# Optimization experiments

Measured on AMD Instinct MI355X. Metric: run time of the kernel, lower is better.

The kernel has to match this reference:

```python
import jax, jax.numpy as jnp
import numpy as np

N_NODES = 100000
N_EDGES = 1600000
F_IN = 128
HIDDEN = 128
N_CLASSES = 32
N_GRAPHS = 64


def setup_inputs() -> dict:
    key = jax.random.key(0)
    ks = jax.random.split(key, 10)
    x = jax.random.normal(ks[0], (N_NODES, F_IN), dtype=jnp.float32)
    edge_index = jax.random.randint(ks[1], (2, N_EDGES), 0, N_NODES, dtype=jnp.int64)
    batch = jnp.sort(jax.random.randint(ks[2], (N_NODES,), 0, N_GRAPHS, dtype=jnp.int64))
    s1 = 1.0 / np.sqrt(F_IN)
    s2 = 1.0 / np.sqrt(HIDDEN)
    W1 = jax.random.normal(ks[3], (F_IN, HIDDEN), dtype=jnp.float32) * s1
    b1 = jnp.zeros((HIDDEN,), dtype=jnp.float32)
    W2 = jax.random.normal(ks[4], (HIDDEN, HIDDEN), dtype=jnp.float32) * s2
    b2 = jnp.zeros((HIDDEN,), dtype=jnp.float32)
    fcW = jax.random.normal(ks[5], (HIDDEN, N_CLASSES), dtype=jnp.float32) * s2
    fcb = jnp.zeros((N_CLASSES,), dtype=jnp.float32)
    return {"x": x, "edge_index": edge_index, "batch": batch,
            "W1": W1, "b1": b1, "W2": W2, "b2": b2, "fcW": fcW, "fcb": fcb}


def _gcn_layer(x, src, dst, W, b, num_nodes):
    # PyG GCNConv: h = X W; out = D^-1/2 (A + I) D^-1/2 h + b,
    # degrees computed over incoming edges at dst, including self-loops.
    h = x @ W  # [N, H]
    ones = jnp.ones(src.shape[0], dtype=x.dtype)
    deg = jax.ops.segment_sum(ones, dst, num_segments=num_nodes) + 1.0  # +1 self-loop
    dinv = jax.lax.rsqrt(deg)  # [N]
    enorm = dinv[src] * dinv[dst]  # [E] per-edge symmetric normalization
    agg = jax.ops.segment_sum(h[src] * enorm[:, None], dst, num_segments=num_nodes)
    agg = agg + h * (dinv * dinv)[:, None]  # self-loop message
    return agg + b


def reference(x, edge_index, batch, W1, b1, W2, b2, fcW, fcb):
    num_nodes = x.shape[0]
    src, dst = edge_index[0], edge_index[1]
    h = jax.nn.relu(_gcn_layer(x, src, dst, W1, b1, num_nodes))
    h = jax.nn.relu(_gcn_layer(h, src, dst, W2, b2, num_nodes))
    # global mean pool per graph
    sums = jax.ops.segment_sum(h, batch, num_segments=N_GRAPHS)  # [G, H]
    cnt = jax.ops.segment_sum(jnp.ones((num_nodes, 1), h.dtype), batch, num_segments=N_GRAPHS)
    pooled = sums / jnp.maximum(cnt, 1.0)
    return pooled @ fcW + fcb  # [G, C]
```

## Files before the change

### kernel.cpp

```cpp
#include <hip/hip_runtime.h>
#include <hip/hip_bf16.h>

#define N_NODES   100000
#define FDIM      128
#define N_GRAPHS  64
#define N_CLASSES 32

#define NB        ((N_NODES + 255) / 256)
#define EPB       8192
#define SCAN_CHUNK 2048

typedef __attribute__((ext_vector_type(8))) short short8;
typedef __attribute__((ext_vector_type(4))) float f32x4;

__device__ __forceinline__ float bf2f(unsigned int u16) {
    unsigned int x = u16 << 16;
    return __builtin_bit_cast(float, x);
}
__device__ __forceinline__ unsigned short f2bf(float f) {
    unsigned int u = __builtin_bit_cast(unsigned int, f);
    unsigned int r = (u + 0x7fffu + ((u >> 16) & 1u)) >> 16;
    return (unsigned short)r;
}

__global__ __launch_bounds__(256) void hist_kernel(const int* __restrict__ dst, int* __restrict__ hist,
                                                   int nE, int nblk) {
    __shared__ int h[NB];
    int t = threadIdx.x, blk = blockIdx.x;
    for (int i = t; i < NB; i += 256) h[i] = 0;
    __syncthreads();
    int base = blk * EPB;
    #pragma unroll
    for (int j = 0; j < EPB / 256; ++j) {
        int e = base + j * 256 + t;
        if (e < nE) atomicAdd(&h[dst[e] >> 8], 1);
    }
    __syncthreads();
    for (int i = t; i < NB; i += 256) hist[i * nblk + blk] = h[i];
}

__global__ __launch_bounds__(256) void scan_p1(const int* __restrict__ a, int* __restrict__ bsums, int n) {
    __shared__ int wsum[4];
    int b = blockIdx.x, t = threadIdx.x;
    int base = b * SCAN_CHUNK;
    int sum = 0;
    #pragma unroll
    for (int j = 0; j < SCAN_CHUNK / 256; ++j) {
        int idx = base + j * 256 + t;
        sum += (idx < n) ? a[idx] : 0;
    }
    #pragma unroll
    for (int off = 32; off; off >>= 1) sum += __shfl_down(sum, off, 64);
    int lane = t & 63, w = t >> 6;
    if (lane == 0) wsum[w] = sum;
    __syncthreads();
    if (t == 0) bsums[b] = wsum[0] + wsum[1] + wsum[2] + wsum[3];
}

__global__ __launch_bounds__(64) void scan_p2(int* __restrict__ bsums, int nb) {
    int t = threadIdx.x;
    int carry = 0;
    for (int base = 0; base < nb; base += 64) {
        int i = base + t;
        int v = (i < nb) ? bsums[i] : 0;
        int inc = v;
        #pragma unroll
        for (int off = 1; off < 64; off <<= 1) {
            int y = __shfl_up(inc, off, 64);
            if (t >= off) inc += y;
        }
        if (i < nb) bsums[i] = carry + inc - v;
        carry += __shfl(inc, 63, 64);
    }
}

__global__ __launch_bounds__(256) void scan_p3(const int* __restrict__ a, const int* __restrict__ bsums,
                                               int* __restrict__ out, int n) {
    __shared__ int wsum[4];
    int b = blockIdx.x, t = threadIdx.x;
    int lane = t & 63, w = t >> 6;
    int i0 = b * SCAN_CHUNK + t * 8;
    int v[8];
    int s = 0;
    #pragma unroll
    for (int j = 0; j < 8; ++j) {
        int idx = i0 + j;
        v[j] = (idx < n) ? a[idx] : 0;
        s += v[j];
    }
    int ps = s;
    #pragma unroll
    for (int off = 1; off < 64; off <<= 1) {
        int y = __shfl_up(ps, off, 64);
        if (lane >= off) ps += y;
    }
    if (lane == 63) wsum[w] = ps;
    __syncthreads();
    if (t == 0) {
        int acc = 0;
        #pragma unroll
        for (int i = 0; i < 4; ++i) { int tmp = wsum[i]; wsum[i] = acc; acc += tmp; }
    }
    __syncthreads();
    int run = (ps - s) + wsum[w] + bsums[b];
    #pragma unroll
    for (int j = 0; j < 8; ++j) {
        int idx = i0 + j;
        if (idx < n) out[idx] = run;
        run += v[j];
    }
}

__global__ __launch_bounds__(256) void part_kernel(const int* __restrict__ src, const int* __restrict__ dst,
                                                   const int* __restrict__ offs,
                                                   unsigned long long* __restrict__ recs,
                                                   int nE, int nblk) {
    __shared__ int cur[NB];
    int t = threadIdx.x, blk = blockIdx.x;
    for (int i = t; i < NB; i += 256) cur[i] = offs[i * nblk + blk];
    __syncthreads();
    int base = blk * EPB;
    #pragma unroll
    for (int j = 0; j < EPB / 256; ++j) {
        int e = base + j * 256 + t;
        if (e < nE) {
            int s = src[e], d = dst[e];
            int pos = atomicAdd(&cur[d >> 8], 1);
            recs[pos] = (unsigned long long)(unsigned)s | ((unsigned long long)(unsigned)d << 32);
        }
    }
}

__global__ __launch_bounds__(256) void csr_kernel(const unsigned long long* __restrict__ recs,
                                                  const int* __restrict__ offs,
                                                  int* __restrict__ row_ptr, int* __restrict__ esrc,
                                                  float* __restrict__ dinv, int nE, int nblk) {
    __shared__ int cnt[256];
    __shared__ int cur[256];
    __shared__ int wsum[4];
    int b = blockIdx.x, t = threadIdx.x;
    int node0 = b << 8;
    int segBeg = offs[b * nblk];
    int segEnd = (b + 1 < NB) ? offs[(b + 1) * nblk] : nE;
    cnt[t] = 0;
    __syncthreads();
    for (int e = segBeg + t; e < segEnd; e += 256) {
        int d = (int)(recs[e] >> 32);
        atomicAdd(&cnt[d - node0], 1);
    }
    __syncthreads();
    int c = cnt[t];
    int lane = t & 63, w = t >> 6;
    int ps = c;
    #pragma unroll
    for (int off = 1; off < 64; off <<= 1) {
        int y = __shfl_up(ps, off, 64);
        if (lane >= off) ps += y;
    }
    if (lane == 63) wsum[w] = ps;
    __syncthreads();
    if (t == 0) {
        int a = 0;
        #pragma unroll
        for (int i = 0; i < 4; ++i) { int tmp = wsum[i]; wsum[i] = a; a += tmp; }
    }
    __syncthreads();
    int gbase = segBeg + (ps - c) + wsum[w];
    cur[t] = gbase;
    int node = node0 + t;
    if (node < N_NODES) {
        row_ptr[node] = gbase;
        dinv[node] = rsqrtf((float)c + 1.0f);
    }
    if (b == NB - 1 && t == 0) row_ptr[N_NODES] = nE;
    __syncthreads();
    for (int e = segBeg + t; e < segEnd; e += 256) {
        unsigned long long r = recs[e];
        int d = (int)(r >> 32);
        int pos = atomicAdd(&cur[d - node0], 1);
        esrc[pos] = (int)(r & 0xffffffffu);
    }
}

__global__ __launch_bounds__(256) void wtrans(const float* __restrict__ W, unsigned short* __restrict__ WT) {
    int idx = blockIdx.x * 256 + threadIdx.x;
    int k = idx >> 7, n = idx & 127;
    WT[n * 128 + k] = f2bf(W[idx]);
}

template<int IN_F32>
__global__ __launch_bounds__(256) void gemm_mfma(const void* __restrict__ Xv,
                                                 const unsigned short* __restrict__ WT,
                                                 unsigned short* __restrict__ H, int nrows) {
    __shared__ char lds[65536];
    char* xs  = lds;
    char* wsh = lds + 32768;
    int t = threadIdx.x;
    int base = blockIdx.x * 128;

    #pragma unroll
    for (int j = 0; j < 8; ++j) {
        int idx = j * 256 + t;
        int n = idx >> 4, c8 = idx & 15;
        short8 v = *(const short8*)(WT + n * 128 + c8 * 8);
        int off = (n * 256 + c8 * 16) ^ ((n & 7) << 4);
        *(short8*)(wsh + off) = v;
    }
    #pragma unroll
    for (int j = 0; j < 8; ++j) {
        int idx = j * 256 + t;
        int row = idx >> 4, c8 = idx & 15;
        int grow = base + row;
        short8 v = {0,0,0,0,0,0,0,0};
        if (grow < nrows) {
            if (IN_F32) {
                const float* Xf = (const float*)Xv;
                float4 a = *(const float4*)(Xf + (size_t)grow * 128 + c8 * 8);
                float4 b = *(const float4*)(Xf + (size_t)grow * 128 + c8 * 8 + 4);
                v[0] = (short)f2bf(a.x); v[1] = (short)f2bf(a.y);
                v[2] = (short)f2bf(a.z); v[3] = (short)f2bf(a.w);
                v[4] = (short)f2bf(b.x); v[5] = (short)f2bf(b.y);
                v[6] = (short)f2bf(b.z); v[7] = (short)f2bf(b.w);
            } else {
                const unsigned short* Xb = (const unsigned short*)Xv;
                v = *(const short8*)(Xb + (size_t)grow * 128 + c8 * 8);
            }
        }
        int off = (row * 256 + c8 * 16) ^ ((row & 7) << 4);
        *(short8*)(xs + off) = v;
    }
    __syncthreads();

    int lane = t & 63, w = t >> 6;
    int lhi = lane >> 4, llo = lane & 15;
    f32x4 acc[2][8];
    #pragma unroll
    for (int r = 0; r < 2; ++r)
        #pragma unroll
        for (int c = 0; c < 8; ++c) acc[r][c] = (f32x4){0.f, 0.f, 0.f, 0.f};

    #pragma unroll
    for (int kk = 0; kk < 4; ++kk) {
        short8 a[2];
        #pragma unroll
        for (int r = 0; r < 2; ++r) {
            int row = w * 32 + r * 16 + llo;
            int off = (row * 256 + kk * 64 + lhi * 16) ^ ((row & 7) << 4);
            a[r] = *(const short8*)(xs + off);
        }
        #pragma unroll
        for (int c = 0; c < 8; ++c) {
            int col = c * 16 + llo;
            int off = (col * 256 + kk * 64 + lhi * 16) ^ ((col & 7) << 4);
            short8 bb = *(const short8*)(wsh + off);
            acc[0][c] = __builtin_amdgcn_mfma_f32_16x16x32_bf16(a[0], bb, acc[0][c], 0, 0, 0);
            acc[1][c] = __builtin_amdgcn_mfma_f32_16x16x32_bf16(a[1], bb, acc[1][c], 0, 0, 0);
        }
    }

    #pragma unroll
    for (int r = 0; r < 2; ++r) {
        #pragma unroll
        for (int reg = 0; reg < 4; ++reg) {
            int grow = base + w * 32 + r * 16 + lhi * 4 + reg;
            if (grow < nrows) {
                #pragma unroll
                for (int c = 0; c < 8; ++c)
                    H[(size_t)grow * 128 + c * 16 + llo] = f2bf(acc[r][c][reg]);
            }
        }
    }
}

__global__ __launch_bounds__(256) void agg_bf16(const unsigned short* __restrict__ H,
                                                unsigned short* __restrict__ O,
                                                const float* __restrict__ dinv,
                                                const int* __restrict__ row_ptr,
                                                const int* __restrict__ esrc,
                                                const float* __restrict__ bias) {
    int node = blockIdx.x * 4 + (threadIdx.x >> 6);
    if (node >= N_NODES) return;
    int lane = threadIdx.x & 63;
    int g  = lane >> 4;
    int fl = lane & 15;

    float dv = dinv[node];
    float acc[8];
    {
        short8 hv = *(const short8*)(H + (size_t)node * FDIM + fl * 8);
        float sw = (g == 0) ? dv * dv : 0.f;
        #pragma unroll
        for (int j = 0; j < 8; ++j) acc[j] = bf2f((unsigned short)hv[j]) * sw;
    }

    int beg = row_ptr[node], end = row_ptr[node + 1];
    for (int e0 = beg; e0 < end; e0 += 4) {
        int e = e0 + g;
        if (e < end) {
            int s = esrc[e];
            float wgt = dinv[s] * dv;
            short8 m = *(const short8*)(H + (size_t)s * FDIM + fl * 8);
            #pragma unroll
            for (int j = 0; j < 8; ++j) acc[j] += bf2f((unsigned short)m[j]) * wgt;
        }
    }

    #pragma unroll
    for (int j = 0; j < 8; ++j) {
        acc[j] += __shfl_xor(acc[j], 16, 64);
        acc[j] += __shfl_xor(acc[j], 32, 64);
    }

    float4 b0 = *(const float4*)(bias + fl * 8);
    float4 b1 = *(const float4*)(bias + fl * 8 + 4);
    float r0 = fmaxf(acc[0] + b0.x, 0.f), r1 = fmaxf(acc[1] + b0.y, 0.f);
    float r2 = fmaxf(acc[2] + b0.z, 0.f), r3 = fmaxf(acc[3] + b0.w, 0.f);
    float r4 = fmaxf(acc[4] + b1.x, 0.f), r5 = fmaxf(acc[5] + b1.y, 0.f);
    float r6 = fmaxf(acc[6] + b1.z, 0.f), r7 = fmaxf(acc[7] + b1.w, 0.f);
    if (g == 0) {
        short8 v;
        v[0] = (short)f2bf(r0); v[1] = (short)f2bf(r1);
        v[2] = (short)f2bf(r2); v[3] = (short)f2bf(r3);
        v[4] = (short)f2bf(r4); v[5] = (short)f2bf(r5);
        v[6] = (short)f2bf(r6); v[7] = (short)f2bf(r7);
        *(short8*)(O + (size_t)node * FDIM + fl * 8) = v;
    }
}

__global__ __launch_bounds__(128) void pool_kernel(const unsigned short* __restrict__ H, const int* __restrict__ batch,
                                                   float* __restrict__ pooled, float* __restrict__ cnt) {
    int f  = threadIdx.x;
    int r0 = blockIdx.x * 128;
    int rend = r0 + 128; if (rend > N_NODES) rend = N_NODES;
    if (r0 >= N_NODES) return;
    float acc = 0.f;
    int g_cur = batch[r0];
    int run = 0;
    for (int r = r0; r < rend; ++r) {
        int g = batch[r];
        if (g != g_cur) {
            atomicAdd(&pooled[g_cur * FDIM + f], acc);
            if (f == 0) atomicAdd(&cnt[g_cur], (float)run);
            acc = 0.f; run = 0; g_cur = g;
        }
        acc += bf2f(H[(size_t)r * FDIM + f]);
        run++;
    }
    atomicAdd(&pooled[g_cur * FDIM + f], acc);
    if (f == 0) atomicAdd(&cnt[g_cur], (float)run);
}

__global__ __launch_bounds__(256) void fc_kernel(const float* __restrict__ pooled, const float* __restrict__ cnt,
                                                 const float* __restrict__ fcW, const float* __restrict__ fcb,
                                                 float* __restrict__ out) {
    int idx = blockIdx.x * 256 + threadIdx.x;
    if (idx >= N_GRAPHS * N_CLASSES) return;
    int g = idx >> 5, c = idx & 31;
    float inv = 1.0f / fmaxf(cnt[g], 1.0f);
    float acc = 0.f;
    #pragma unroll 16
    for (int k = 0; k < FDIM; ++k) acc += pooled[g * FDIM + k] * fcW[k * N_CLASSES + c];
    out[idx] = acc * inv + fcb[c];
}

extern "C" void kernel_launch(void* const* d_in, const int* in_sizes, int n_in,
                              void* d_out, int out_size, void* d_ws, size_t ws_size,
                              hipStream_t stream) {
    const float* x    = (const float*)d_in[0];
    const int*   ei   = (const int*)d_in[1];
    const int*   batch= (const int*)d_in[2];
    const float* W1   = (const float*)d_in[3];
    const float* b1   = (const float*)d_in[4];
    const float* W2   = (const float*)d_in[5];
    const float* b2   = (const float*)d_in[6];
    const float* fcW  = (const float*)d_in[7];
    const float* fcb  = (const float*)d_in[8];
    float* out = (float*)d_out;

    const int nE = in_sizes[1] / 2;
    const int* src = ei;
    const int* dst = ei + nE;

    const int nblk  = (nE + EPB - 1) / EPB;
    const int histN = NB * nblk;
    const int sB    = (histN + SCAN_CHUNK - 1) / SCAN_CHUNK;

    unsigned short* Hb0 = (unsigned short*)d_ws;
    unsigned short* Hb1 = Hb0 + (size_t)N_NODES * FDIM;
    unsigned short* W1T = Hb1 + (size_t)N_NODES * FDIM;
    unsigned short* W2T = W1T + FDIM * FDIM;
    float* dinv    = (float*)(W2T + FDIM * FDIM);
    int*   row_ptr = (int*)(dinv + N_NODES);
    int*   esrc    = row_ptr + N_NODES + 1;
    unsigned long long* recs = (unsigned long long*)(esrc + ((nE + 1) & ~1));
    int*   hist    = (int*)(recs + nE);
    int*   bsums   = hist + histN;
    float* pooled  = (float*)(bsums + ((sB + 1) & ~1));
    float* cnt     = pooled + N_GRAPHS * FDIM;

    hipMemsetAsync(pooled, 0, (N_GRAPHS * FDIM + N_GRAPHS) * sizeof(float), stream);

    wtrans<<<64, 256, 0, stream>>>(W1, W1T);
    wtrans<<<64, 256, 0, stream>>>(W2, W2T);

    hist_kernel<<<nblk, 256, 0, stream>>>(dst, hist, nE, nblk);
    scan_p1<<<sB, 256, 0, stream>>>(hist, bsums, histN);
    scan_p2<<<1, 64, 0, stream>>>(bsums, sB);
    scan_p3<<<sB, 256, 0, stream>>>(hist, bsums, hist, histN);
    part_kernel<<<nblk, 256, 0, stream>>>(src, dst, hist, recs, nE, nblk);
    csr_kernel<<<NB, 256, 0, stream>>>(recs, hist, row_ptr, esrc, dinv, nE, nblk);

    const int gemm_grid = (N_NODES + 127) / 128;
    gemm_mfma<1><<<gemm_grid, 256, 0, stream>>>(x, W1T, Hb0, N_NODES);
    agg_bf16<<<(N_NODES + 3) / 4, 256, 0, stream>>>(Hb0, Hb1, dinv, row_ptr, esrc, b1);
    gemm_mfma<0><<<gemm_grid, 256, 0, stream>>>(Hb1, W2T, Hb0, N_NODES);
    agg_bf16<<<(N_NODES + 3) / 4, 256, 0, stream>>>(Hb0, Hb1, dinv, row_ptr, esrc, b2);

    pool_kernel<<<(N_NODES + 127) / 128, 128, 0, stream>>>(Hb1, batch, pooled, cnt);
    fc_kernel<<<(N_GRAPHS * N_CLASSES + 255) / 256, 256, 0, stream>>>(pooled, cnt, fcW, fcb, out);
}
```

Measured before the change: 404.2 us.

## Store features in 16-column chunk-major layout and aggregate per column chunk

```diff
diff --git a/kernel.cpp b/kernel.cpp
--- a/kernel.cpp
+++ b/kernel.cpp
@@ -9,6 +9,7 @@
 #define NB        ((N_NODES + 255) / 256)
 #define EPB       8192
 #define SCAN_CHUNK 2048
+#define CHS       ((size_t)N_NODES * 16)
 
 typedef __attribute__((ext_vector_type(8))) short short8;
 typedef __attribute__((ext_vector_type(4))) float f32x4;
@@ -165,14 +166,17 @@
         for (int i = 0; i < 4; ++i) { int tmp = wsum[i]; wsum[i] = a; a += tmp; }
     }
     __syncthreads();
-    int gbase = segBeg + (ps - c) + wsum[w];
-    cur[t] = gbase;
     int node = node0 + t;
+    int rbase = segBeg + node0 + (ps - c) + wsum[w] + t;
     if (node < N_NODES) {
-        row_ptr[node] = gbase;
+        row_ptr[node] = rbase;
+        esrc[rbase] = node;
         dinv[node] = rsqrtf((float)c + 1.0f);
-    }
-    if (b == NB - 1 && t == 0) row_ptr[N_NODES] = nE;
+        cur[t] = rbase + 1;
+    } else {
+        cur[t] = 0;
+    }
+    if (b == NB - 1 && t == 0) row_ptr[N_NODES] = nE + N_NODES;
     __syncthreads();
     for (int e = segBeg + t; e < segEnd; e += 256) {
         unsigned long long r = recs[e];
@@ -223,7 +227,7 @@
                 v[6] = (short)f2bf(b.z); v[7] = (short)f2bf(b.w);
             } else {
                 const unsigned short* Xb = (const unsigned short*)Xv;
-                v = *(const short8*)(Xb + (size_t)grow * 128 + c8 * 8);
+                v = *(const short8*)(Xb + (size_t)(c8 >> 1) * CHS + (size_t)grow * 16 + (c8 & 1) * 8);
             }
         }
         int off = (row * 256 + c8 * 16) ^ ((row & 7) << 4);
@@ -266,7 +270,7 @@
             if (grow < nrows) {
                 #pragma unroll
                 for (int c = 0; c < 8; ++c)
-                    H[(size_t)grow * 128 + c * 16 + llo] = f2bf(acc[r][c][reg]);
+                    H[(size_t)c * CHS + (size_t)grow * 16 + llo] = f2bf(acc[r][c][reg]);
             }
         }
     }
@@ -278,58 +282,65 @@
                                                 const int* __restrict__ row_ptr,
                                                 const int* __restrict__ esrc,
                                                 const float* __restrict__ bias) {
-    int node = blockIdx.x * 4 + (threadIdx.x >> 6);
-    if (node >= N_NODES) return;
-    int lane = threadIdx.x & 63;
-    int g  = lane >> 4;
-    int fl = lane & 15;
+    int cm  = blockIdx.x & 7;
+    int grp = blockIdx.x >> 3;
+    int t = threadIdx.x;
+    int node = grp * 16 + (t >> 4);
+    int slot = (t >> 1) & 7;
+    int h    = t & 1;
+    const unsigned short* Hc = H + (size_t)cm * CHS;
 
     float dv = dinv[node];
     float acc[8];
-    {
-        short8 hv = *(const short8*)(H + (size_t)node * FDIM + fl * 8);
-        float sw = (g == 0) ? dv * dv : 0.f;
-        #pragma unroll
-        for (int j = 0; j < 8; ++j) acc[j] = bf2f((unsigned short)hv[j]) * sw;
-    }
+    #pragma unroll
+    for (int j = 0; j < 8; ++j) acc[j] = 0.f;
 
     int beg = row_ptr[node], end = row_ptr[node + 1];
-    for (int e0 = beg; e0 < end; e0 += 4) {
-        int e = e0 + g;
-        if (e < end) {
-            int s = esrc[e];
-            float wgt = dinv[s] * dv;
-            short8 m = *(const short8*)(H + (size_t)s * FDIM + fl * 8);
-            #pragma unroll
-            for (int j = 0; j < 8; ++j) acc[j] += bf2f((unsigned short)m[j]) * wgt;
-        }
+    for (int e0 = beg; e0 < end; e0 += 16) {
+        int ea = e0 + slot;
+        int eb = ea + 8;
+        int ca = min(ea, end - 1);
+        int cb = min(eb, end - 1);
+        int s0 = esrc[ca];
+        int s1 = esrc[cb];
+        float w0 = (ea < end) ? dinv[s0] * dv : 0.f;
+        float w1 = (eb < end) ? dinv[s1] * dv : 0.f;
+        short8 m0 = *(const short8*)(Hc + (size_t)s0 * 16 + h * 8);
+        short8 m1 = *(const short8*)(Hc + (size_t)s1 * 16 + h * 8);
+        #pragma unroll
+        for (int j = 0; j < 8; ++j) acc[j] += bf2f((unsigned short)m0[j]) * w0;
+        #pragma unroll
+        for (int j = 0; j < 8; ++j) acc[j] += bf2f((unsigned short)m1[j]) * w1;
     }
 
     #pragma unroll
     for (int j = 0; j < 8; ++j) {
-        acc[j] += __shfl_xor(acc[j], 16, 64);
-        acc[j] += __shfl_xor(acc[j], 32, 64);
-    }
-
-    float4 b0 = *(const float4*)(bias + fl * 8);
-    float4 b1 = *(const float4*)(bias + fl * 8 + 4);
-    float r0 = fmaxf(acc[0] + b0.x, 0.f), r1 = fmaxf(acc[1] + b0.y, 0.f);
-    float r2 = fmaxf(acc[2] + b0.z, 0.f), r3 = fmaxf(acc[3] + b0.w, 0.f);
-    float r4 = fmaxf(acc[4] + b1.x, 0.f), r5 = fmaxf(acc[5] + b1.y, 0.f);
-    float r6 = fmaxf(acc[6] + b1.z, 0.f), r7 = fmaxf(acc[7] + b1.w, 0.f);
-    if (g == 0) {
+        acc[j] += __shfl_xor(acc[j], 2, 64);
+        acc[j] += __shfl_xor(acc[j], 4, 64);
+        acc[j] += __shfl_xor(acc[j], 8, 64);
+    }
+
+    if (slot == 0) {
+        int fb = cm * 16 + h * 8;
+        float4 b0 = *(const float4*)(bias + fb);
+        float4 b1 = *(const float4*)(bias + fb + 4);
         short8 v;
-        v[0] = (short)f2bf(r0); v[1] = (short)f2bf(r1);
-        v[2] = (short)f2bf(r2); v[3] = (short)f2bf(r3);
-        v[4] = (short)f2bf(r4); v[5] = (short)f2bf(r5);
-        v[6] = (short)f2bf(r6); v[7] = (short)f2bf(r7);
-        *(short8*)(O + (size_t)node * FDIM + fl * 8) = v;
+        v[0] = (short)f2bf(fmaxf(acc[0] + b0.x, 0.f));
+        v[1] = (short)f2bf(fmaxf(acc[1] + b0.y, 0.f));
+        v[2] = (short)f2bf(fmaxf(acc[2] + b0.z, 0.f));
+        v[3] = (short)f2bf(fmaxf(acc[3] + b0.w, 0.f));
+        v[4] = (short)f2bf(fmaxf(acc[4] + b1.x, 0.f));
+        v[5] = (short)f2bf(fmaxf(acc[5] + b1.y, 0.f));
+        v[6] = (short)f2bf(fmaxf(acc[6] + b1.z, 0.f));
+        v[7] = (short)f2bf(fmaxf(acc[7] + b1.w, 0.f));
+        *(short8*)(O + (size_t)cm * CHS + (size_t)node * 16 + h * 8) = v;
     }
 }
 
 __global__ __launch_bounds__(128) void pool_kernel(const unsigned short* __restrict__ H, const int* __restrict__ batch,
                                                    float* __restrict__ pooled, float* __restrict__ cnt) {
     int f  = threadIdx.x;
+    size_t faddr = (size_t)(f >> 4) * CHS + (f & 15);
     int r0 = blockIdx.x * 128;
     int rend = r0 + 128; if (rend > N_NODES) rend = N_NODES;
     if (r0 >= N_NODES) return;
@@ -343,7 +354,7 @@
             if (f == 0) atomicAdd(&cnt[g_cur], (float)run);
             acc = 0.f; run = 0; g_cur = g;
         }
-        acc += bf2f(H[(size_t)r * FDIM + f]);
+        acc += bf2f(H[faddr + (size_t)r * 16]);
         run++;
     }
     atomicAdd(&pooled[g_cur * FDIM + f], acc);
@@ -384,6 +395,7 @@
     const int nblk  = (nE + EPB - 1) / EPB;
     const int histN = NB * nblk;
     const int sB    = (histN + SCAN_CHUNK - 1) / SCAN_CHUNK;
+    const int nSlots = nE + N_NODES;
 
     unsigned short* Hb0 = (unsigned short*)d_ws;
     unsigned short* Hb1 = Hb0 + (size_t)N_NODES * FDIM;
@@ -392,7 +404,7 @@
     float* dinv    = (float*)(W2T + FDIM * FDIM);
     int*   row_ptr = (int*)(dinv + N_NODES);
     int*   esrc    = row_ptr + N_NODES + 1;
-    unsigned long long* recs = (unsigned long long*)(esrc + ((nE + 1) & ~1));
+    unsigned long long* recs = (unsigned long long*)(esrc + ((nSlots + 1) & ~1));
     int*   hist    = (int*)(recs + nE);
     int*   bsums   = hist + histN;
     float* pooled  = (float*)(bsums + ((sB + 1) & ~1));
@@ -411,10 +423,11 @@
     csr_kernel<<<NB, 256, 0, stream>>>(recs, hist, row_ptr, esrc, dinv, nE, nblk);
 
     const int gemm_grid = (N_NODES + 127) / 128;
+    const int agg_grid  = (N_NODES / 16) * 8;
     gemm_mfma<1><<<gemm_grid, 256, 0, stream>>>(x, W1T, Hb0, N_NODES);
-    agg_bf16<<<(N_NODES + 3) / 4, 256, 0, stream>>>(Hb0, Hb1, dinv, row_ptr, esrc, b1);
+    agg_bf16<<<agg_grid, 256, 0, stream>>>(Hb0, Hb1, dinv, row_ptr, esrc, b1);
     gemm_mfma<0><<<gemm_grid, 256, 0, stream>>>(Hb1, W2T, Hb0, N_NODES);
-    agg_bf16<<<(N_NODES + 3) / 4, 256, 0, stream>>>(Hb0, Hb1, dinv, row_ptr, esrc, b2);
+    agg_bf16<<<agg_grid, 256, 0, stream>>>(Hb0, Hb1, dinv, row_ptr, esrc, b2);
 
     pool_kernel<<<(N_NODES + 127) / 128, 128, 0, stream>>>(Hb1, batch, pooled, cnt);
     fc_kernel<<<(N_GRAPHS * N_CLASSES + 255) / 256, 256, 0, stream>>>(pooled, cnt, fcW, fcb, out);
```

Result: slower. 480.3 us (+18.8%).
